# Kernel tuning notes

Hardware: AMD Instinct MI355X
Metric: run time of the kernel (lower is better)

Reference implementation:

```python
import jax, jax.numpy as jnp
import numpy as np
import math

D_MODEL, D_STATE, D_CONV, EXPAND = 1024, 64, 4, 2
D_INNER = EXPAND * D_MODEL
DT_RANK = math.ceil(D_MODEL / 8)
B_SZ, L_SEQ = 2, 4096


def setup_inputs() -> dict:
    key = jax.random.key(0)
    ks = jax.random.split(key, 8)
    hidden_states = jax.random.normal(ks[0], (B_SZ, L_SEQ, D_MODEL), jnp.float32)
    in_proj_w = jax.random.normal(ks[1], (2 * D_INNER, D_MODEL), jnp.float32) * (D_MODEL ** -0.5)
    conv_w = jax.random.normal(ks[2], (D_INNER, 1, D_CONV), jnp.float32) * (D_CONV ** -0.5)
    conv_b = jnp.zeros((D_INNER,), jnp.float32)
    x_proj_w = jax.random.normal(ks[3], (DT_RANK + 2 * D_STATE, D_INNER), jnp.float32) * (D_INNER ** -0.5)
    dt_init_std = DT_RANK ** -0.5
    dt_proj_w = jax.random.uniform(ks[4], (D_INNER, DT_RANK), jnp.float32, -dt_init_std, dt_init_std)
    # inverse-softplus init of dt bias, as in the torch module
    dt = jnp.exp(jax.random.uniform(ks[5], (D_INNER,), jnp.float32) * (math.log(0.1) - math.log(0.001)) + math.log(0.001))
    dt = jnp.clip(dt, 1e-4, None)
    dt_proj_b = dt + jnp.log(-jnp.expm1(-dt))
    A_log = jnp.log(jnp.broadcast_to(jnp.arange(1, D_STATE + 1, dtype=jnp.float32), (D_INNER, D_STATE)))
    D = jnp.ones((D_INNER,), jnp.float32)
    out_proj_w = jax.random.normal(ks[6], (D_MODEL, D_INNER), jnp.float32) * (D_INNER ** -0.5)
    return dict(hidden_states=hidden_states, in_proj_w=in_proj_w, conv_w=conv_w, conv_b=conv_b,
                x_proj_w=x_proj_w, dt_proj_w=dt_proj_w, dt_proj_b=dt_proj_b,
                A_log=A_log, D=D, out_proj_w=out_proj_w)


def _mamba_fwd(hidden_states, in_proj_w, conv_w, conv_b, x_proj_w, dt_proj_w, dt_proj_b, A_log, D, out_proj_w):
    b, l, _ = hidden_states.shape
    d_inner, d_state = A_log.shape
    dt_rank = dt_proj_w.shape[1]
    xz = hidden_states @ in_proj_w.T                      # (b, l, 2*d_inner)
    x, z = xz[..., :d_inner], xz[..., d_inner:]
    # causal depthwise conv over time
    xc = jax.lax.conv_general_dilated(
        x.transpose(0, 2, 1), conv_w, window_strides=(1,),
        padding=[(conv_w.shape[-1] - 1, 0)],
        dimension_numbers=('NCH', 'OIH', 'NCH'),
        feature_group_count=d_inner) + conv_b[None, :, None]
    x = jax.nn.silu(xc).transpose(0, 2, 1)                # (b, l, d_inner)
    x_dbl = x @ x_proj_w.T                                # (b, l, dt_rank + 2*d_state)
    dt_low = x_dbl[..., :dt_rank]
    Bmat = x_dbl[..., dt_rank:dt_rank + d_state]          # (b, l, n)
    Cmat = x_dbl[..., dt_rank + d_state:]                 # (b, l, n)
    dt = jax.nn.softplus(dt_low @ dt_proj_w.T + dt_proj_b)  # (b, l, d_inner)
    A = -jnp.exp(A_log)                                   # (d_inner, n)

    def step(h, inp):
        x_t, dt_t, B_t, C_t = inp                         # (b,d), (b,d), (b,n), (b,n)
        dA = jnp.exp(dt_t[..., None] * A)                 # (b, d, n)
        h = h * dA + (dt_t * x_t)[..., None] * B_t[:, None, :]
        y = jnp.einsum('bdn,bn->bd', h, C_t)
        return h, y

    xs = (x.transpose(1, 0, 2), dt.transpose(1, 0, 2), Bmat.transpose(1, 0, 2), Cmat.transpose(1, 0, 2))
    h0 = jnp.zeros((b, d_inner, d_state), x.dtype)
    _, ys = jax.lax.scan(step, h0, xs)                    # (l, b, d_inner)
    y = ys.transpose(1, 0, 2) + D * x
    y = y * jax.nn.silu(z)
    return y @ out_proj_w.T                               # (b, l, d_model)


def reference(hidden_states, in_proj_w, conv_w, conv_b, x_proj_w, dt_proj_w, dt_proj_b, A_log, D, out_proj_w):
    return _mamba_fwd(hidden_states, in_proj_w, conv_w, conv_b, x_proj_w, dt_proj_w, dt_proj_b, A_log, D, out_proj_w)
```

## Files before the change

### kernel.cpp

```cpp
#include <hip/hip_runtime.h>
#include <math.h>

#define B_SZ 2
#define L_SEQ 4096
#define D_MODEL 1024
#define D_INNER 2048
#define D_STATE 64
#define DT_RANK 128
#define BL (B_SZ * L_SEQ)

#define AS1 __attribute__((address_space(1)))
#define AS3 __attribute__((address_space(3)))

typedef __attribute__((ext_vector_type(8))) short bf16x8_t;
typedef __attribute__((ext_vector_type(4))) float f32x4_t;
typedef __attribute__((ext_vector_type(2))) unsigned int u32x2_t;

__device__ __forceinline__ unsigned short f2bf(float f) {
    unsigned int u = __float_as_uint(f);
    u = (u + 0x7FFFu + ((u >> 16) & 1u)) >> 16;
    return (unsigned short)u;
}
__device__ __forceinline__ float bf2f(unsigned short h) {
    return __uint_as_float(((unsigned int)h) << 16);
}

__global__ __launch_bounds__(256) void cvt_f32_bf16(
    const float* __restrict__ in, unsigned short* __restrict__ out, int n4)
{
    int i = blockIdx.x * 256 + threadIdx.x;
    if (i >= n4) return;
    float4 v = ((const float4*)in)[i];
    ushort4 o;
    o.x = f2bf(v.x); o.y = f2bf(v.y); o.z = f2bf(v.z); o.w = f2bf(v.w);
    ((ushort4*)out)[i] = o;
}

__global__ __launch_bounds__(256) void cvt_dtpart(
    const float* __restrict__ xdbl, unsigned short* __restrict__ out)
{
    int i = blockIdx.x * 256 + threadIdx.x;
    int m = i >> 5, c = i & 31;
    float4 v = *(const float4*)(xdbl + (size_t)m * 256 + c * 4);
    ushort4 o;
    o.x = f2bf(v.x); o.y = f2bf(v.y); o.z = f2bf(v.z); o.w = f2bf(v.w);
    ((ushort4*)(out))[(size_t)m * 32 + c] = o;
}

__global__ __launch_bounds__(256) void gemm_bf16(
    const unsigned short* __restrict__ A, int lda,
    const unsigned short* __restrict__ B, int ldb,
    float* __restrict__ C, int ldc, int K,
    const float* __restrict__ bias, int act)
{
    __shared__ unsigned short As[128 * 32];
    __shared__ unsigned short Bs[128 * 32];

    const int tid = threadIdx.x;
    const int w = tid >> 6, lane = tid & 63;
    const int bm = blockIdx.y * 128, bn = blockIdx.x * 128;
    const int wm = (w & 1) * 64, wn = (w >> 1) * 64;

    f32x4_t acc[4][4];
#pragma unroll
    for (int i = 0; i < 4; ++i)
#pragma unroll
        for (int j = 0; j < 4; ++j) acc[i][j] = (f32x4_t){0.f, 0.f, 0.f, 0.f};

    const int srow = lane >> 2;
    const int scol = (lane & 3) * 8;
    const unsigned short* Ag0 = A + (size_t)(bm + w * 16 + srow) * lda + scol;
    const unsigned short* Ag1 = A + (size_t)(bm + 64 + w * 16 + srow) * lda + scol;
    const unsigned short* Bg0 = B + (size_t)(bn + w * 16 + srow) * ldb + scol;
    const unsigned short* Bg1 = B + (size_t)(bn + 64 + w * 16 + srow) * ldb + scol;
    unsigned short* la0 = &As[(w * 16) * 32];
    unsigned short* la1 = &As[(64 + w * 16) * 32];
    unsigned short* lb0 = &Bs[(w * 16) * 32];
    unsigned short* lb1 = &Bs[(64 + w * 16) * 32];

    const int fr = lane & 15;
    const int fk = (lane >> 4) * 8;

    for (int k0 = 0; k0 < K; k0 += 32) {
        __syncthreads();
        __builtin_amdgcn_global_load_lds((const AS1 void*)(Ag0 + k0), (AS3 void*)la0, 16, 0, 0);
        __builtin_amdgcn_global_load_lds((const AS1 void*)(Ag1 + k0), (AS3 void*)la1, 16, 0, 0);
        __builtin_amdgcn_global_load_lds((const AS1 void*)(Bg0 + k0), (AS3 void*)lb0, 16, 0, 0);
        __builtin_amdgcn_global_load_lds((const AS1 void*)(Bg1 + k0), (AS3 void*)lb1, 16, 0, 0);
        __syncthreads();

        bf16x8_t af[4], bfr[4];
#pragma unroll
        for (int i = 0; i < 4; ++i)
            af[i] = *(const bf16x8_t*)&As[(wm + i * 16 + fr) * 32 + fk];
#pragma unroll
        for (int j = 0; j < 4; ++j)
            bfr[j] = *(const bf16x8_t*)&Bs[(wn + j * 16 + fr) * 32 + fk];
#pragma unroll
        for (int i = 0; i < 4; ++i)
#pragma unroll
            for (int j = 0; j < 4; ++j)
                acc[i][j] = __builtin_amdgcn_mfma_f32_16x16x32_bf16(
                    af[i], bfr[j], acc[i][j], 0, 0, 0);
    }

    const int erow = (lane >> 4) * 4;
    const int ecol = lane & 15;
#pragma unroll
    for (int i = 0; i < 4; ++i) {
        int gr0 = bm + wm + i * 16 + erow;
#pragma unroll
        for (int j = 0; j < 4; ++j) {
            int gc = bn + wn + j * 16 + ecol;
#pragma unroll
            for (int r = 0; r < 4; ++r) {
                float v = acc[i][j][r];
                if (act == 1) {
                    float t = v + bias[gr0 + r];
                    v = (t > 20.f) ? t : log1pf(__expf(t));
                } else if (act == 2) {
                    v = v / (1.f + __expf(-v));
                }
                C[(size_t)(gr0 + r) * ldc + gc] = v;
            }
        }
    }
}

__global__ __launch_bounds__(256) void conv_silu_kernel(
    const float* __restrict__ xT,
    const float* __restrict__ w,
    const float* __restrict__ bias,
    unsigned short* __restrict__ xcT16)
{
    int gid = blockIdx.x * blockDim.x + threadIdx.x;
    int d = gid >> 11;
    int c4 = gid & 2047;
    int m0 = c4 * 4;
    int l0 = m0 & (L_SEQ - 1);

    const float* row = xT + (size_t)d * BL;
    float4 v = *(const float4*)(row + m0);
    float4 p;
    if (l0 == 0) { p.x = p.y = p.z = p.w = 0.f; }
    else         { p = *(const float4*)(row + m0 - 4); }

    float4 wv = ((const float4*)w)[d];
    float bb = bias[d];
    float e[4];
    e[0] = bb + wv.x * p.y + wv.y * p.z + wv.z * p.w + wv.w * v.x;
    e[1] = bb + wv.x * p.z + wv.y * p.w + wv.z * v.x + wv.w * v.y;
    e[2] = bb + wv.x * p.w + wv.y * v.x + wv.z * v.y + wv.w * v.z;
    e[3] = bb + wv.x * v.x + wv.y * v.y + wv.z * v.z + wv.w * v.w;
    ushort4 o;
    o.x = f2bf(e[0] / (1.f + __expf(-e[0])));
    o.y = f2bf(e[1] / (1.f + __expf(-e[1])));
    o.z = f2bf(e[2] / (1.f + __expf(-e[2])));
    o.w = f2bf(e[3] / (1.f + __expf(-e[3])));
    ((ushort4*)(xcT16 + (size_t)d * BL))[c4] = o;
}

__global__ __launch_bounds__(256) void transpose_f32_bf16(
    const float* __restrict__ in, int ldin,
    unsigned short* __restrict__ out, int ldout)
{
    __shared__ float tl[32][33];
    int r0 = blockIdx.y * 32, c0 = blockIdx.x * 32;
    int tx = threadIdx.x & 31, ty = threadIdx.x >> 5;
#pragma unroll
    for (int k = 0; k < 4; ++k)
        tl[ty + 8 * k][tx] = in[(size_t)(r0 + ty + 8 * k) * ldin + c0 + tx];
    __syncthreads();
#pragma unroll
    for (int k = 0; k < 4; ++k)
        out[(size_t)(c0 + ty + 8 * k) * ldout + r0 + tx] = f2bf(tl[tx][ty + 8 * k]);
}

__global__ __launch_bounds__(256) void transpose_bf16(
    const unsigned short* __restrict__ in, int ldin,
    unsigned short* __restrict__ out, int ldout)
{
    __shared__ unsigned short tl[32][33];
    int r0 = blockIdx.y * 32, c0 = blockIdx.x * 32;
    int tx = threadIdx.x & 31, ty = threadIdx.x >> 5;
#pragma unroll
    for (int k = 0; k < 4; ++k)
        tl[ty + 8 * k][tx] = in[(size_t)(r0 + ty + 8 * k) * ldin + c0 + tx];
    __syncthreads();
#pragma unroll
    for (int k = 0; k < 4; ++k)
        out[(size_t)(c0 + ty + 8 * k) * ldout + r0 + tx] = tl[tx][ty + 8 * k];
}

#define SCHUNK 512
#define WSTEPS 32

#if __has_builtin(__builtin_amdgcn_permlane32_swap)
#define HAVE_PL32 1
__device__ __forceinline__ float pl32_fold(float x, float y) {
    u32x2_t r = __builtin_amdgcn_permlane32_swap(
        __float_as_uint(x), __float_as_uint(y), false, false);
    return __uint_as_float(r.x) + __uint_as_float(r.y);
}
#endif
#if __has_builtin(__builtin_amdgcn_permlane16_swap)
#define HAVE_PL16 1
__device__ __forceinline__ float pl16_fold(float x, float y) {
    u32x2_t r = __builtin_amdgcn_permlane16_swap(
        __float_as_uint(x), __float_as_uint(y), false, false);
    return __uint_as_float(r.x) + __uint_as_float(r.y);
}
#endif

#ifdef HAVE_PL32
#define FOLD_STAGE1                                                          \
    if (dir32) {                                                             \
        _Pragma("unroll")                                                    \
        for (int t = 0; t < 8; ++t) pr[t] = pl32_fold(pr[t + 8], pr[t]);     \
    } else {                                                                 \
        _Pragma("unroll")                                                    \
        for (int t = 0; t < 8; ++t) pr[t] = pl32_fold(pr[t], pr[t + 8]);     \
    }
#else
#define FOLD_STAGE1                                                          \
    _Pragma("unroll")                                                        \
    for (int t = 0; t < 8; ++t) {                                            \
        float send = (lane & 32) ? pr[t] : pr[t + 8];                        \
        float recv = __shfl_xor(send, 32);                                   \
        pr[t] = ((lane & 32) ? pr[t + 8] : pr[t]) + recv;                    \
    }
#endif

#ifdef HAVE_PL16
#define FOLD_STAGE2                                                          \
    if (dir16) {                                                             \
        _Pragma("unroll")                                                    \
        for (int t = 0; t < 4; ++t) pr[t] = pl16_fold(pr[t + 4], pr[t]);     \
    } else {                                                                 \
        _Pragma("unroll")                                                    \
        for (int t = 0; t < 4; ++t) pr[t] = pl16_fold(pr[t], pr[t + 4]);     \
    }
#else
#define FOLD_STAGE2                                                          \
    _Pragma("unroll")                                                        \
    for (int t = 0; t < 4; ++t) {                                            \
        float send = (lane & 16) ? pr[t] : pr[t + 4];                        \
        float recv = __shfl_xor(send, 16);                                   \
        pr[t] = ((lane & 16) ? pr[t + 4] : pr[t]) + recv;                    \
    }
#endif

#if __has_builtin(__builtin_amdgcn_mov_dpp)
#define BFLY21                                                               \
    pr[0] += __int_as_float(__builtin_amdgcn_mov_dpp(                        \
                 __float_as_int(pr[0]), 0x4E, 0xF, 0xF, true));              \
    pr[0] += __int_as_float(__builtin_amdgcn_mov_dpp(                        \
                 __float_as_int(pr[0]), 0xB1, 0xF, 0xF, true));
#else
#define BFLY21                                                               \
    pr[0] += __shfl_xor(pr[0], 2);                                           \
    pr[0] += __shfl_xor(pr[0], 1);
#endif

#define STAGE_BC(W, DB)                                                      \
{                                                                            \
    const unsigned t0_ = (unsigned)(W) * WSTEPS;                             \
    _Pragma("unroll")                                                        \
    for (int r_ = 0; r_ < 2; ++r_) {                                         \
        const int sl_ = r_ * 16 + wid * 2;                                   \
        const float* src_ = xdbl + (size_t)(bL + t0_ + sl_ + (lane >> 5)) * 256 \
                            + DT_RANK + (lane & 31) * 4;                     \
        __builtin_amdgcn_global_load_lds((const AS1 void*)src_,              \
            (AS3 void*)&s_bc[DB][sl_][0], 16, 0, 0);                         \
    }                                                                        \
}

#define GROUP16(GG2)                                                         \
{                                                                            \
    const int gp = gpos + (GG2);                 \
    const int zi = cbase + gp + myt16;    \
    float zv = 0.f;                                                          \
    if ((lane & 3) == 0) zv = zrow[zi];     \
    float Bv[16], Cv[16];                                                    \
    _Pragma("unroll")                                                        \
    for (int t = 0; t < 16; ++t) {                                           \
        Bv[t] = sbcw[((GG2) + t) * 128 + lane];                              \
        Cv[t] = sbcw[((GG2) + t) * 128 + 64 + lane];                         \
    }                                                                        \
    float4 dta = *(const float4*)&sdt[gp];                                   \
    float4 dtb = *(const float4*)&sdt[gp + 4];                               \
    float4 dtc = *(const float4*)&sdt[gp + 8];                               \
    float4 dtd = *(const float4*)&sdt[gp + 12];                              \
    float4 dxa = *(const float4*)&sdtx[gp];                                  \
    float4 dxb = *(const float4*)&sdtx[gp + 4];                              \
    float4 dxc = *(const float4*)&sdtx[gp + 8];                              \
    float4 dxd = *(const float4*)&sdtx[gp + 12];                             \
    float dt16[16] = {dta.x, dta.y, dta.z, dta.w, dtb.x, dtb.y, dtb.z, dtb.w,\
                      dtc.x, dtc.y, dtc.z, dtc.w, dtd.x, dtd.y, dtd.z, dtd.w};\
    float dx16[16] = {dxa.x, dxa.y, dxa.z, dxa.w, dxb.x, dxb.y, dxb.z, dxb.w,\
                      dxc.x, dxc.y, dxc.z, dxc.w, dxd.x, dxd.y, dxd.z, dxd.w};\
    float pr[16];                                                            \
    _Pragma("unroll")                                                        \
    for (int t = 0; t < 16; ++t) {                                           \
        float a = __builtin_amdgcn_exp2f(dt16[t] * An2);                     \
        h = fmaf(h, a, dx16[t] * Bv[t]);                                     \
        pr[t] = h * Cv[t];                                                   \
    }                                                                        \
    FOLD_STAGE1;                                                             \
    FOLD_STAGE2;                                                             \
    _Pragma("unroll")                                                        \
    for (int t = 0; t < 2; ++t) {                     \
        float send = (lane & 8) ? pr[t] : pr[t + 2];                         \
        float recv = __shfl_xor(send, 8);                                    \
        pr[t] = ((lane & 8) ? pr[t + 2] : pr[t]) + recv;                     \
    }                                                                        \
    {                                                 \
        float send = (lane & 4) ? pr[0] : pr[1];                             \
        float recv = __shfl_xor(send, 4);                                    \
        pr[0] = ((lane & 4) ? pr[1] : pr[0]) + recv;                         \
    }                                                                        \
    BFLY21;                                 \
    if ((lane & 3) == 0) {               \
        float xv = bf2f(sx[gp + myt16]);                                     \
        zrow[zi] = fmaf(Dd, xv, pr[0]) * zv;                                 \
    }                                                                        \
}

__global__ __launch_bounds__(512, 4) void scan_seq_kernel(
    const float* __restrict__ dtT,
    const unsigned short* __restrict__ xcT16,
    const float* __restrict__ xdbl,
    float* __restrict__ zyT,
    const float* __restrict__ A_log,
    const float* __restrict__ Dp)
{
    __shared__ __align__(16) float s_dt[8][SCHUNK];
    __shared__ __align__(16) float s_dtx[8][SCHUNK];
    __shared__ __align__(16) unsigned short s_x[8][SCHUNK];
    __shared__ __align__(16) float s_bc[2][WSTEPS][128];

    const int tid  = threadIdx.x;
    const int wid  = tid >> 6;
    const int lane = tid & 63;
    const int bi   = blockIdx.x;
    const int b    = bi & 1;
    const int d    = (bi >> 1) * 8 + wid;
    const int bL   = b * L_SEQ;

    const size_t rowbase = (size_t)d * BL + (size_t)bL;
    const float An2 = -__expf(A_log[d * D_STATE + lane]) * 1.44269504f;
    const float Dd  = Dp[d];

#ifdef HAVE_PL32
    bool dir32;
    {
        u32x2_t r = __builtin_amdgcn_permlane32_swap((unsigned)lane,
                        (unsigned)lane + 1000u, false, false);
        dir32 = (__builtin_amdgcn_readfirstlane(r.x) == 1032u);
    }
#endif
#ifdef HAVE_PL16
    bool dir16;
    {
        u32x2_t r = __builtin_amdgcn_permlane16_swap((unsigned)lane,
                        (unsigned)lane + 1000u, false, false);
        dir16 = (__builtin_amdgcn_readfirstlane(r.x) == 1016u);
    }
#endif

    float* sdt = s_dt[wid];
    float* sdtx = s_dtx[wid];
    unsigned short* sx = s_x[wid];
    const float* dtrow = dtT + rowbase;
    const unsigned short* xrow = xcT16 + rowbase;
    float* zrow = zyT + rowbase;
    const int myt16 = (lane >> 2) & 15;

    float4 pA = ((const float4*)dtrow)[2 * lane];
    float4 pB = ((const float4*)dtrow)[2 * lane + 1];
    uint4  pX = ((const uint4*)xrow)[lane];

    float h = 0.f;
    int buf = 0;

    STAGE_BC(0, 0);
    __syncthreads();

    for (int c = 0; c < L_SEQ / SCHUNK; ++c) {
        ((float4*)sdt)[2 * lane]     = pA;
        ((float4*)sdt)[2 * lane + 1] = pB;
        ((uint4*)sx)[lane]           = pX;
        float4 dxA, dxB;
        dxA.x = pA.x * __uint_as_float(pX.x << 16);
        dxA.y = pA.y * __uint_as_float(pX.x & 0xffff0000u);
        dxA.z = pA.z * __uint_as_float(pX.y << 16);
        dxA.w = pA.w * __uint_as_float(pX.y & 0xffff0000u);
        dxB.x = pB.x * __uint_as_float(pX.z << 16);
        dxB.y = pB.y * __uint_as_float(pX.z & 0xffff0000u);
        dxB.z = pB.z * __uint_as_float(pX.w << 16);
        dxB.w = pB.w * __uint_as_float(pX.w & 0xffff0000u);
        ((float4*)sdtx)[2 * lane]     = dxA;
        ((float4*)sdtx)[2 * lane + 1] = dxB;

        if (c < L_SEQ / SCHUNK - 1) {
            pA = ((const float4*)(dtrow + (c + 1) * SCHUNK))[2 * lane];
            pB = ((const float4*)(dtrow + (c + 1) * SCHUNK))[2 * lane + 1];
            pX = ((const uint4*)(xrow + (c + 1) * SCHUNK))[lane];
        }
        const int cbase = c * SCHUNK;

        for (int wd = 0; wd < SCHUNK / WSTEPS; ++wd) {
            const int wglob = c * (SCHUNK / WSTEPS) + wd;
            if (wglob + 1 < L_SEQ / WSTEPS)
                STAGE_BC(wglob + 1, buf ^ 1);
            const int gpos = wd * WSTEPS;
            const float* sbcw = &s_bc[buf][0][0];
            GROUP16(0);
            GROUP16(16);
            __syncthreads();
            buf ^= 1;
        }
    }
}

extern "C" void kernel_launch(void* const* d_in, const int* in_sizes, int n_in,
                              void* d_out, int out_size, void* d_ws, size_t ws_size,
                              hipStream_t stream)
{
    const float* hs        = (const float*)d_in[0];
    const float* in_proj_w = (const float*)d_in[1];
    const float* conv_w    = (const float*)d_in[2];
    const float* conv_b    = (const float*)d_in[3];
    const float* x_proj_w  = (const float*)d_in[4];
    const float* dt_proj_w = (const float*)d_in[5];
    const float* dt_proj_b = (const float*)d_in[6];
    const float* A_log     = (const float*)d_in[7];
    const float* Dp        = (const float*)d_in[8];
    const float* out_proj_w= (const float*)d_in[9];
    float* out = (float*)d_out;

    char* ws = (char*)d_ws;
    const size_t MiB = 1024 * 1024;
    float*          xT    = (float*)(ws);
    unsigned short* xc16  = (unsigned short*)(ws);
    float*          dtT   = (float*)(ws);
    float*          zT    = (float*)(ws + 64 * MiB);
    unsigned short* W1_16 = (unsigned short*)(ws + 128 * MiB);
    unsigned short* hs16  = (unsigned short*)(ws + 136 * MiB);
    unsigned short* xcT16 = (unsigned short*)(ws + 128 * MiB);
    unsigned short* y16   = (unsigned short*)(ws + 128 * MiB);
    float*          xdbl  = (float*)(ws + 160 * MiB);
    unsigned short* xdbl16= (unsigned short*)(ws + 169 * MiB);
    unsigned short* Wx16  = (unsigned short*)(ws + 171 * MiB);
    unsigned short* Wdt16 = (unsigned short*)(ws + 172 * MiB);
    unsigned short* Wo16  = (unsigned short*)(ws + 173 * MiB);

    dim3 blk(256);

    cvt_f32_bf16<<<8192, blk, 0, stream>>>(hs, hs16, 2097152);
    cvt_f32_bf16<<<4096, blk, 0, stream>>>(in_proj_w, W1_16, 1048576);
    cvt_f32_bf16<<<512, blk, 0, stream>>>(x_proj_w, Wx16, 131072);
    cvt_f32_bf16<<<256, blk, 0, stream>>>(dt_proj_w, Wdt16, 65536);
    cvt_f32_bf16<<<2048, blk, 0, stream>>>(out_proj_w, Wo16, 524288);

    gemm_bf16<<<dim3(64, 16), blk, 0, stream>>>(
        W1_16, D_MODEL, hs16, D_MODEL, xT, BL, D_MODEL, nullptr, 0);

    gemm_bf16<<<dim3(64, 16), blk, 0, stream>>>(
        W1_16 + (size_t)D_INNER * D_MODEL, D_MODEL, hs16, D_MODEL,
        zT, BL, D_MODEL, nullptr, 2);

    conv_silu_kernel<<<(D_INNER * (BL / 4)) / 256, blk, 0, stream>>>(
        xT, conv_w, conv_b, xcT16);

    transpose_bf16<<<dim3(BL / 32, D_INNER / 32), blk, 0, stream>>>(
        xcT16, BL, xc16, D_INNER);

    gemm_bf16<<<dim3(2, 64), blk, 0, stream>>>(
        xc16, D_INNER, Wx16, D_INNER, xdbl, 256, D_INNER, nullptr, 0);

    cvt_dtpart<<<1024, blk, 0, stream>>>(xdbl, xdbl16);

    gemm_bf16<<<dim3(64, 16), blk, 0, stream>>>(
        Wdt16, DT_RANK, xdbl16, DT_RANK, dtT, BL, DT_RANK, dt_proj_b, 1);

    scan_seq_kernel<<<512, dim3(512), 0, stream>>>(
        dtT, xcT16, xdbl, zT, A_log, Dp);

    transpose_f32_bf16<<<dim3(BL / 32, D_INNER / 32), blk, 0, stream>>>(
        zT, BL, y16, D_INNER);

    gemm_bf16<<<dim3(8, 64), blk, 0, stream>>>(
        y16, D_INNER, Wo16, D_INNER, out, D_MODEL, D_INNER, nullptr, 0);
}
```

Baseline: 862.8 us.

## Repack B/C into time-interleaved layout for vectorized LDS reads in scan

Adds a repack kernel that rewrites the B and C columns of x_dbl so each state's values for four consecutive timesteps sit contiguously. The scan kernel then stages this layout into shared memory and reads B/C as float4 per lane, replacing 32 scalar LDS loads per 16-step group with 8 vector loads. It also hoists the z loads for both 16-step groups ahead of the compute. The cost is an extra kernel launch plus about 8 MB of extra global traffic. The repacked buffer reuses workspace regions whose earlier contents are no longer needed.

```diff
diff --git a/kernel.cpp b/kernel.cpp
--- a/kernel.cpp
+++ b/kernel.cpp
@@ -45,6 +45,18 @@
     ushort4 o;
     o.x = f2bf(v.x); o.y = f2bf(v.y); o.z = f2bf(v.z); o.w = f2bf(v.w);
     ((ushort4*)(out))[(size_t)m * 32 + c] = o;
+}
+
+__global__ __launch_bounds__(256) void repack_bc(
+    const float* __restrict__ xdbl,
+    float* __restrict__ bc2)
+{
+    int i = blockIdx.x * 256 + threadIdx.x;
+    int t4 = i >> 7, n = i & 127;
+    const float* s = xdbl + (size_t)(t4 * 4) * 256 + 128 + n;
+    float4 o;
+    o.x = s[0]; o.y = s[256]; o.z = s[512]; o.w = s[768];
+    ((float4*)bc2)[i] = o;
 }
 
 __global__ __launch_bounds__(256) void gemm_bf16(
@@ -264,28 +276,24 @@
 
 #define STAGE_BC(W, DB)                                                      \
 {                                                                            \
-    const unsigned t0_ = (unsigned)(W) * WSTEPS;                             \
+    const float* wbase_ = bc2 + (size_t)(bQ + 8u * (unsigned)(W)) * 512;     \
     _Pragma("unroll")                                                        \
     for (int r_ = 0; r_ < 2; ++r_) {                                         \
-        const int sl_ = r_ * 16 + wid * 2;                                   \
-        const float* src_ = xdbl + (size_t)(bL + t0_ + sl_ + (lane >> 5)) * 256 \
-                            + DT_RANK + (lane & 31) * 4;                     \
+        const float* src_ = wbase_ + (wid * 2 + r_) * 256 + lane * 4;        \
         __builtin_amdgcn_global_load_lds((const AS1 void*)src_,              \
-            (AS3 void*)&s_bc[DB][sl_][0], 16, 0, 0);                         \
+            (AS3 void*)&s_bc2[DB][(wid * 2 + r_) * 256], 16, 0, 0);          \
     }                                                                        \
 }
 
-#define GROUP16(GG2)                                                         \
+#define GROUP16(GG2, ZV)                                                     \
 {                                                                            \
     const int gp = gpos + (GG2);                 \
-    const int zi = cbase + gp + myt16;    \
-    float zv = 0.f;                                                          \
-    if ((lane & 3) == 0) zv = zrow[zi];     \
-    float Bv[16], Cv[16];                                                    \
+    const int t4b = (GG2) >> 2;                                              \
+    f32x4_t bv[4], cv[4];                                                    \
     _Pragma("unroll")                                                        \
-    for (int t = 0; t < 16; ++t) {                                           \
-        Bv[t] = sbcw[((GG2) + t) * 128 + lane];                              \
-        Cv[t] = sbcw[((GG2) + t) * 128 + 64 + lane];                         \
+    for (int a = 0; a < 4; ++a) {       \
+        bv[a] = *(const f32x4_t*)&sbcw[(t4b + a) * 512 + lane * 4];          \
+        cv[a] = *(const f32x4_t*)&sbcw[(t4b + a) * 512 + 256 + lane * 4];    \
     }                                                                        \
     float4 dta = *(const float4*)&sdt[gp];                                   \
     float4 dtb = *(const float4*)&sdt[gp + 4];                               \
@@ -302,9 +310,9 @@
     float pr[16];                                                            \
     _Pragma("unroll")                                                        \
     for (int t = 0; t < 16; ++t) {                                           \
-        float a = __builtin_amdgcn_exp2f(dt16[t] * An2);                     \
-        h = fmaf(h, a, dx16[t] * Bv[t]);                                     \
-        pr[t] = h * Cv[t];                                                   \
+        float a_ = __builtin_amdgcn_exp2f(dt16[t] * An2);                    \
+        h = fmaf(h, a_, dx16[t] * bv[t >> 2][t & 3]);                        \
+        pr[t] = h * cv[t >> 2][t & 3];                                       \
     }                                                                        \
     FOLD_STAGE1;                                                             \
     FOLD_STAGE2;                                                             \
@@ -322,14 +330,14 @@
     BFLY21;                                 \
     if ((lane & 3) == 0) {               \
         float xv = bf2f(sx[gp + myt16]);                                     \
-        zrow[zi] = fmaf(Dd, xv, pr[0]) * zv;                                 \
+        zrow[cbase + gp + myt16] = fmaf(Dd, xv, pr[0]) * (ZV);               \
     }                                                                        \
 }
 
 __global__ __launch_bounds__(512, 4) void scan_seq_kernel(
     const float* __restrict__ dtT,
     const unsigned short* __restrict__ xcT16,
-    const float* __restrict__ xdbl,
+    const float* __restrict__ bc2,
     float* __restrict__ zyT,
     const float* __restrict__ A_log,
     const float* __restrict__ Dp)
@@ -337,7 +345,7 @@
     __shared__ __align__(16) float s_dt[8][SCHUNK];
     __shared__ __align__(16) float s_dtx[8][SCHUNK];
     __shared__ __align__(16) unsigned short s_x[8][SCHUNK];
-    __shared__ __align__(16) float s_bc[2][WSTEPS][128];
+    __shared__ __align__(16) float s_bc2[2][WSTEPS * 128];
 
     const int tid  = threadIdx.x;
     const int wid  = tid >> 6;
@@ -345,9 +353,9 @@
     const int bi   = blockIdx.x;
     const int b    = bi & 1;
     const int d    = (bi >> 1) * 8 + wid;
-    const int bL   = b * L_SEQ;
-
-    const size_t rowbase = (size_t)d * BL + (size_t)bL;
+    const unsigned bQ = (unsigned)b * (L_SEQ / 4);
+
+    const size_t rowbase = (size_t)d * BL + (size_t)(b * L_SEQ);
     const float An2 = -__expf(A_log[d * D_STATE + lane]) * 1.44269504f;
     const float Dd  = Dp[d];
 
@@ -414,9 +422,14 @@
             if (wglob + 1 < L_SEQ / WSTEPS)
                 STAGE_BC(wglob + 1, buf ^ 1);
             const int gpos = wd * WSTEPS;
-            const float* sbcw = &s_bc[buf][0][0];
-            GROUP16(0);
-            GROUP16(16);
+            float zv0 = 0.f, zv1 = 0.f;
+            if ((lane & 3) == 0) {
+                zv0 = zrow[cbase + gpos + myt16];
+                zv1 = zrow[cbase + gpos + 16 + myt16];
+            }
+            const float* sbcw = s_bc2[buf];
+            GROUP16(0, zv0);
+            GROUP16(16, zv1);
             __syncthreads();
             buf ^= 1;
         }
@@ -451,6 +464,7 @@
     unsigned short* y16   = (unsigned short*)(ws + 128 * MiB);
     float*          xdbl  = (float*)(ws + 160 * MiB);
     unsigned short* xdbl16= (unsigned short*)(ws + 169 * MiB);
+    float*          bc2   = (float*)(ws + 169 * MiB);
     unsigned short* Wx16  = (unsigned short*)(ws + 171 * MiB);
     unsigned short* Wdt16 = (unsigned short*)(ws + 172 * MiB);
     unsigned short* Wo16  = (unsigned short*)(ws + 173 * MiB);
@@ -484,8 +498,10 @@
     gemm_bf16<<<dim3(64, 16), blk, 0, stream>>>(
         Wdt16, DT_RANK, xdbl16, DT_RANK, dtT, BL, DT_RANK, dt_proj_b, 1);
 
+    repack_bc<<<1024, blk, 0, stream>>>(xdbl, bc2);
+
     scan_seq_kernel<<<512, dim3(512), 0, stream>>>(
-        dtT, xcT16, xdbl, zT, A_log, Dp);
+        dtT, xcT16, bc2, zT, A_log, Dp);
 
     transpose_f32_bf16<<<dim3(BL / 32, D_INNER / 32), blk, 0, stream>>>(
         zT, BL, y16, D_INNER);
```

Result: no change. 847.4 us (-1.8%).
